# Kernel optimization log

Measured on AMD Instinct MI355X. Metric: run time of the kernel, lower is better.

Reference implementation:

```python
import jax, jax.numpy as jnp
import numpy as np
from jax import lax

DN = ('NCHW', 'OIHW', 'NCHW')

def conv2d(x, w, b):
    # valid cross-correlation, identical math to torch Conv2d / the module's
    # flattened-FFT circular-conv + roll(1) + crop trick
    y = lax.conv_general_dilated(x, w, window_strides=(1, 1), padding='VALID',
                                 dimension_numbers=DN)
    return y + b[None, :, None, None]

def max_pool2(x):
    return lax.reduce_window(x, -jnp.inf, lax.max,
                             window_dimensions=(1, 1, 2, 2),
                             window_strides=(1, 1, 2, 2), padding='VALID')

def setup_inputs() -> dict:
    key = jax.random.key(0)
    ks = jax.random.split(key, 9)
    B = 2048
    x = jax.random.normal(ks[0], (B, 1, 28, 28), dtype=jnp.float32)
    s = 0.05
    w1 = jax.random.normal(ks[1], (32, 1, 3, 3), dtype=jnp.float32) * s
    b1 = jax.random.normal(ks[2], (32,), dtype=jnp.float32) * s
    w2 = jax.random.normal(ks[3], (64, 32, 3, 3), dtype=jnp.float32) * s
    b2 = jax.random.normal(ks[4], (64,), dtype=jnp.float32) * s
    fc1_w = jax.random.normal(ks[5], (128, 9216), dtype=jnp.float32) * 0.01
    fc1_b = jax.random.normal(ks[6], (128,), dtype=jnp.float32) * s
    fc2_w = jax.random.normal(ks[7], (10, 128), dtype=jnp.float32) * s
    fc2_b = jax.random.normal(ks[8], (10,), dtype=jnp.float32) * s
    return {'x': x, 'w1': w1, 'b1': b1, 'w2': w2, 'b2': b2,
            'fc1_w': fc1_w, 'fc1_b': fc1_b, 'fc2_w': fc2_w, 'fc2_b': fc2_b}

def reference(x, w1, b1, w2, b2, fc1_w, fc1_b, fc2_w, fc2_b):
    h = jax.nn.relu(conv2d(x, w1, b1))           # [B,32,26,26]
    h = jax.nn.relu(conv2d(h, w2, b2))           # [B,64,24,24]
    h = max_pool2(h)                             # [B,64,12,12]
    # dropout layers are identity at inference
    h = h.reshape(h.shape[0], -1)                # [B,9216]
    h = jax.nn.relu(h @ fc1_w.T + fc1_b)         # [B,128]
    logits = h @ fc2_w.T + fc2_b                 # [B,10]
    # NB: original forward returns x (pre-log_softmax logits), not `output`
    return logits
```

## Files before the change

kernel.cpp:

```cpp
#include <hip/hip_runtime.h>
#include <stddef.h>


#define NIMG 2048

typedef __attribute__((ext_vector_type(8))) short short8;
typedef __attribute__((ext_vector_type(4))) float f32x4;

__device__ inline ushort f2bf(float f) {
    unsigned u = __builtin_bit_cast(unsigned, f);
    unsigned r = (u + 0x7fff + ((u >> 16) & 1)) >> 16;
    return (ushort)r;
}

__global__ void k_w2pack(const float* __restrict__ w2, ushort* __restrict__ bfr) {
    int i = blockIdx.x * 256 + threadIdx.x;
    if (i < 18432) {
        int j = i & 7;
        int l = (i >> 3) & 63;
        int t = i >> 9;
        int kyx = t % 9, nt = t / 9;
        int oc = nt * 16 + (l & 15);
        int ic = 8 * (l >> 4) + j;
        bfr[i] = f2bf(w2[oc * 288 + ic * 9 + kyx]);
    }
}

__global__ void k_fc1wpack(const float* __restrict__ fc1_w, ushort* __restrict__ wp) {
    int idx = blockIdx.x * 256 + threadIdx.x;
    if (idx < 128 * 9216) {
        int n = idx / 9216, kp = idx % 9216;
        int j = kp & 1;
        int lane = (kp >> 1) & 63;
        int t = kp >> 7;
        int i = t % 9, wv = t / 9;
        int oc = (2 * (wv & 1) + j) * 16 + (lane & 15);
        int mt = (wv >> 1) + i * 4;
        int qid = mt * 4 + (lane >> 4);
        wp[idx] = f2bf(fc1_w[(size_t)n * 9216 + oc * 144 + qid]);
    }
}

#define SWZB(q, g) ((((q) << 6) | ((g) << 4)) ^ (((q) & 14) << 3))

__launch_bounds__(512)
__global__ void k_conv_fused(const float* __restrict__ x,
                             const float* __restrict__ w1,
                             const float* __restrict__ b1,
                             const ushort* __restrict__ bfr,
                             const float* __restrict__ b2,
                             ushort* __restrict__ pooled) {
    __shared__ char smem[46400];
    float* xs = (float*)(smem + 43264);
    const int tid = threadIdx.x;
    const int img = blockIdx.x;
    const int lane = tid & 63;
    const int w = tid >> 6;

    const float* xg = x + (size_t)img * 784;
    for (int i = tid; i < 784; i += 512) xs[i] = xg[i];

    const int ocg = tid & 3;
    float w1r[72], b1r[8];
    #pragma unroll
    for (int j = 0; j < 8; j++) {
        b1r[j] = b1[ocg * 8 + j];
        #pragma unroll
        for (int q = 0; q < 9; q++) w1r[j * 9 + q] = w1[(ocg * 8 + j) * 9 + q];
    }
    __syncthreads();

    #pragma unroll
    for (int it = 0; it < 3; it++) {
        int pid = (tid >> 2) + it * 128;
        if (pid < 338) {
            int y = pid / 13;
            int px2 = (pid - y * 13) * 2;
            const float* xr = &xs[y * 28 + px2];
            float xv[3][4];
            #pragma unroll
            for (int r = 0; r < 3; r++) {
                float2 u = *(const float2*)&xr[r * 28];
                float2 v = *(const float2*)&xr[r * 28 + 2];
                xv[r][0] = u.x; xv[r][1] = u.y; xv[r][2] = v.x; xv[r][3] = v.y;
            }
            short8 pk0, pk1;
            #pragma unroll
            for (int j = 0; j < 8; j++) {
                float s0 = b1r[j], s1 = b1r[j];
                #pragma unroll
                for (int ky = 0; ky < 3; ky++)
                    #pragma unroll
                    for (int kx = 0; kx < 3; kx++) {
                        float wv = w1r[j * 9 + ky * 3 + kx];
                        s0 = fmaf(wv, xv[ky][kx], s0);
                        s1 = fmaf(wv, xv[ky][kx + 1], s1);
                    }
                pk0[j] = (short)f2bf(fmaxf(s0, 0.0f));
                pk1[j] = (short)f2bf(fmaxf(s1, 0.0f));
            }
            int pos0 = y * 26 + px2;
            *(short8*)(smem + SWZB(pos0, ocg)) = pk0;
            *(short8*)(smem + SWZB(pos0 + 1, ocg)) = pk1;
        }
    }
    __syncthreads();

    const int p = w & 1;
    const int g = w >> 1;

    short8 bf[2][9];
    #pragma unroll
    for (int j = 0; j < 2; j++)
        #pragma unroll
        for (int kyx = 0; kyx < 9; kyx++)
            bf[j][kyx] = *(const short8*)&bfr[(((2 * p + j) * 9 + kyx) * 64 + lane) * 8];

    const int row = lane & 15;
    const int ic8 = lane >> 4;
    float b2v[2];
    b2v[0] = b2[(2 * p) * 16 + row];
    b2v[1] = b2[(2 * p + 1) * 16 + row];

    unsigned* pp = (unsigned*)(pooled + (size_t)img * 9216);

    #pragma unroll 1
    for (int i = 0; i < 9; i++) {
        int mt = g + i * 4;
        int m = mt * 16 + row;
        int qid = m >> 2;
        int de = m & 3;
        int py = qid / 12, px = qid - py * 12;
        int yy = py * 2 + (de >> 1);
        int xx2 = px * 2 + (de & 1);
        int pos = yy * 26 + xx2;

        f32x4 acc0 = {0.f, 0.f, 0.f, 0.f};
        f32x4 acc1 = {0.f, 0.f, 0.f, 0.f};
        #pragma unroll
        for (int ky = 0; ky < 3; ky++)
            #pragma unroll
            for (int kx = 0; kx < 3; kx++) {
                int q = pos + ky * 26 + kx;
                short8 a = *(const short8*)(smem + SWZB(q, ic8));
                acc0 = __builtin_amdgcn_mfma_f32_16x16x32_bf16(a, bf[0][ky * 3 + kx], acc0, 0, 0, 0);
                acc1 = __builtin_amdgcn_mfma_f32_16x16x32_bf16(a, bf[1][ky * 3 + kx], acc1, 0, 0, 0);
            }
        float v0 = fmaxf(fmaxf(fmaxf(acc0[0], acc0[1]), fmaxf(acc0[2], acc0[3])) + b2v[0], 0.0f);
        float v1 = fmaxf(fmaxf(fmaxf(acc1[0], acc1[1]), fmaxf(acc1[2], acc1[3])) + b2v[1], 0.0f);
        pp[(w * 9 + i) * 64 + lane] = (unsigned)f2bf(v0) | ((unsigned)f2bf(v1) << 16);
    }
}

#define FC1_SPLIT 16
#define FC1_CHUNK 576

__launch_bounds__(512)
__global__ void k_fc1(const ushort* __restrict__ A,
                      const ushort* __restrict__ Wp,
                      float* __restrict__ part) {
    __shared__ ushort As[128 * 64];
    __shared__ ushort Ws[128 * 64];
    char* Ac = (char*)As;
    char* Wc = (char*)Ws;

    const int t = threadIdx.x;
    const int lane = t & 63;
    const int wv = t >> 6;
    const int wm = wv >> 2;
    const int wn = wv & 3;
    const int lr = lane & 15;
    const int lk = lane >> 4;
    const int m0 = blockIdx.x * 128;
    const int kc0 = blockIdx.y * FC1_CHUNK;

    const int trow = t >> 2;
    const int seg = t & 3;
    const int wb0 = trow * 128 + seg * 32;
    const int sw = (trow & 7) << 4;

    const ushort* Ab = A + (size_t)(m0 + trow) * 9216 + kc0 + seg * 16;
    const ushort* Wb = Wp + (size_t)trow * 9216 + kc0 + seg * 16;

    f32x4 acc[4][2];
    #pragma unroll
    for (int mf = 0; mf < 4; mf++)
        #pragma unroll
        for (int nf = 0; nf < 2; nf++) acc[mf][nf] = (f32x4){0.f, 0.f, 0.f, 0.f};

    short8 ra0 = *(const short8*)(Ab);
    short8 ra1 = *(const short8*)(Ab + 8);
    short8 rw0 = *(const short8*)(Wb);
    short8 rw1 = *(const short8*)(Wb + 8);
    short8 na0, na1, nw0, nw1;

    for (int s = 0; s < 9; s++) {
        *(short8*)(Ac + (wb0 ^ sw)) = ra0;
        *(short8*)(Ac + ((wb0 + 16) ^ sw)) = ra1;
        *(short8*)(Wc + (wb0 ^ sw)) = rw0;
        *(short8*)(Wc + ((wb0 + 16) ^ sw)) = rw1;
        __syncthreads();
        if (s < 8) {
            const ushort* An = Ab + (s + 1) * 64;
            const ushort* Wn = Wb + (s + 1) * 64;
            na0 = *(const short8*)(An);
            na1 = *(const short8*)(An + 8);
            nw0 = *(const short8*)(Wn);
            nw1 = *(const short8*)(Wn + 8);
        }
        #pragma unroll
        for (int ks = 0; ks < 2; ks++) {
            short8 af[4], bfr2[2];
            #pragma unroll
            for (int mf = 0; mf < 4; mf++) {
                int r = wm * 64 + mf * 16 + lr;
                af[mf] = *(const short8*)(Ac + ((r * 128 + ks * 64 + lk * 16) ^ ((r & 7) << 4)));
            }
            #pragma unroll
            for (int nf = 0; nf < 2; nf++) {
                int n = wn * 32 + nf * 16 + lr;
                bfr2[nf] = *(const short8*)(Wc + ((n * 128 + ks * 64 + lk * 16) ^ ((n & 7) << 4)));
            }
            #pragma unroll
            for (int mf = 0; mf < 4; mf++)
                #pragma unroll
                for (int nf = 0; nf < 2; nf++)
                    acc[mf][nf] = __builtin_amdgcn_mfma_f32_16x16x32_bf16(af[mf], bfr2[nf], acc[mf][nf], 0, 0, 0);
        }
        __syncthreads();
        if (s < 8) { ra0 = na0; ra1 = na1; rw0 = nw0; rw1 = nw1; }
    }

    float* pb = part + (size_t)blockIdx.y * (2048 * 128);
    #pragma unroll
    for (int mf = 0; mf < 4; mf++)
        #pragma unroll
        for (int nf = 0; nf < 2; nf++) {
            int mrow = m0 + wm * 64 + mf * 16 + lk * 4;
            int ncol = wn * 32 + nf * 16 + lr;
            #pragma unroll
            for (int q = 0; q < 4; q++)
                pb[(size_t)(mrow + q) * 128 + ncol] = acc[mf][nf][q];
        }
}

__global__ void k_fc2(const float* __restrict__ part,
                      const float* __restrict__ fc1_b,
                      const float* __restrict__ fc2_w,
                      const float* __restrict__ fc2_b,
                      float* __restrict__ out) {
    __shared__ float hs[16 * 128];
    __shared__ float wsm[10 * 128];
    __shared__ float bsm[10];
    const int t = threadIdx.x;
    const int m0 = blockIdx.x * 16;
    for (int i = t; i < 1280; i += 256) wsm[i] = fc2_w[i];
    if (t < 10) bsm[t] = fc2_b[t];
    #pragma unroll
    for (int e = 0; e < 8; e++) {
        int i = t + e * 256;
        int r = i >> 7, c = i & 127;
        float s = fc1_b[c];
        #pragma unroll
        for (int kc = 0; kc < FC1_SPLIT; kc++)
            s += part[(size_t)kc * (2048 * 128) + (size_t)(m0 + r) * 128 + c];
        hs[i] = fmaxf(s, 0.0f);
    }
    __syncthreads();
    int r = t / 16, c = t % 16;
    if (c < 10) {
        float s = bsm[c];
        const float* hp = &hs[r * 128];
        const float* wp = &wsm[c * 128];
        #pragma unroll
        for (int k = 0; k < 128; k++) s = fmaf(hp[k], wp[k], s);
        out[(size_t)(m0 + r) * 10 + c] = s;
    }
}

extern "C" void kernel_launch(void* const* d_in, const int* in_sizes, int n_in,
                              void* d_out, int out_size, void* d_ws, size_t ws_size,
                              hipStream_t stream) {
    const float* x     = (const float*)d_in[0];
    const float* w1    = (const float*)d_in[1];
    const float* b1    = (const float*)d_in[2];
    const float* w2    = (const float*)d_in[3];
    const float* b2    = (const float*)d_in[4];
    const float* fc1_w = (const float*)d_in[5];
    const float* fc1_b = (const float*)d_in[6];
    const float* fc2_w = (const float*)d_in[7];
    const float* fc2_b = (const float*)d_in[8];
    float* out = (float*)d_out;

    char* wsb = (char*)d_ws;
    ushort* bfr    = (ushort*)wsb;
    ushort* wp     = (ushort*)(wsb + 36864);
    ushort* pooled = (ushort*)(wsb + 2396160);
    float*  part   = (float*)(wsb + 40144896);

    k_w2pack<<<72, 256, 0, stream>>>(w2, bfr);
    k_fc1wpack<<<4608, 256, 0, stream>>>(fc1_w, wp);
    k_conv_fused<<<NIMG, 512, 0, stream>>>(x, w1, b1, bfr, b2, pooled);
    k_fc1<<<dim3(16, FC1_SPLIT), 512, 0, stream>>>(pooled, wp, part);
    k_fc2<<<NIMG / 16, 256, 0, stream>>>(part, fc1_b, fc2_w, fc2_b, out);
}
```

Before: 99.73 us.

## Split conv2 output tiles into sequential passes, drop LDS swizzle, raise occupancy hint

The conv2 MFMA loop now handles the two output-channel tiles one after the other instead of together, so only 9 B fragments are live at a time. This lowers VGPR pressure, and the launch bound now requests 6 blocks per SM. The first tile's pooled results are kept in a small array and packed into the output on the second pass. The XOR swizzle on the conv1 LDS layout is removed for plain linear addressing. Risks: more LDS bank conflicts, A fragments read twice, less MFMA interleaving, and `pv0[i]` indexed inside a non-unrolled loop may be placed in scratch memory. The occupancy hint may also cause spills, while LDS use alone already caps residency at about 3 blocks.

```diff
diff --git a/kernel.cpp b/kernel.cpp
--- a/kernel.cpp
+++ b/kernel.cpp
@@ -41,9 +41,7 @@
     }
 }
 
-#define SWZB(q, g) ((((q) << 6) | ((g) << 4)) ^ (((q) & 14) << 3))
-
-__launch_bounds__(512)
+__launch_bounds__(512, 6)
 __global__ void k_conv_fused(const float* __restrict__ x,
                              const float* __restrict__ w1,
                              const float* __restrict__ b1,
@@ -100,55 +98,55 @@
                 pk1[j] = (short)f2bf(fmaxf(s1, 0.0f));
             }
             int pos0 = y * 26 + px2;
-            *(short8*)(smem + SWZB(pos0, ocg)) = pk0;
-            *(short8*)(smem + SWZB(pos0 + 1, ocg)) = pk1;
+            *(short8*)(smem + pos0 * 64 + ocg * 16) = pk0;
+            *(short8*)(smem + (pos0 + 1) * 64 + ocg * 16) = pk1;
         }
     }
     __syncthreads();
 
     const int p = w & 1;
     const int g = w >> 1;
-
-    short8 bf[2][9];
-    #pragma unroll
-    for (int j = 0; j < 2; j++)
-        #pragma unroll
-        for (int kyx = 0; kyx < 9; kyx++)
-            bf[j][kyx] = *(const short8*)&bfr[(((2 * p + j) * 9 + kyx) * 64 + lane) * 8];
-
     const int row = lane & 15;
     const int ic8 = lane >> 4;
-    float b2v[2];
-    b2v[0] = b2[(2 * p) * 16 + row];
-    b2v[1] = b2[(2 * p + 1) * 16 + row];
 
     unsigned* pp = (unsigned*)(pooled + (size_t)img * 9216);
+    float pv0[9];
 
     #pragma unroll 1
-    for (int i = 0; i < 9; i++) {
-        int mt = g + i * 4;
-        int m = mt * 16 + row;
-        int qid = m >> 2;
-        int de = m & 3;
-        int py = qid / 12, px = qid - py * 12;
-        int yy = py * 2 + (de >> 1);
-        int xx2 = px * 2 + (de & 1);
-        int pos = yy * 26 + xx2;
-
-        f32x4 acc0 = {0.f, 0.f, 0.f, 0.f};
-        f32x4 acc1 = {0.f, 0.f, 0.f, 0.f};
-        #pragma unroll
-        for (int ky = 0; ky < 3; ky++)
-            #pragma unroll
-            for (int kx = 0; kx < 3; kx++) {
-                int q = pos + ky * 26 + kx;
-                short8 a = *(const short8*)(smem + SWZB(q, ic8));
-                acc0 = __builtin_amdgcn_mfma_f32_16x16x32_bf16(a, bf[0][ky * 3 + kx], acc0, 0, 0, 0);
-                acc1 = __builtin_amdgcn_mfma_f32_16x16x32_bf16(a, bf[1][ky * 3 + kx], acc1, 0, 0, 0);
-            }
-        float v0 = fmaxf(fmaxf(fmaxf(acc0[0], acc0[1]), fmaxf(acc0[2], acc0[3])) + b2v[0], 0.0f);
-        float v1 = fmaxf(fmaxf(fmaxf(acc1[0], acc1[1]), fmaxf(acc1[2], acc1[3])) + b2v[1], 0.0f);
-        pp[(w * 9 + i) * 64 + lane] = (unsigned)f2bf(v0) | ((unsigned)f2bf(v1) << 16);
+    for (int nt = 0; nt < 2; nt++) {
+        short8 bfv[9];
+        #pragma unroll
+        for (int kyx = 0; kyx < 9; kyx++)
+            bfv[kyx] = *(const short8*)&bfr[(((2 * p + nt) * 9 + kyx) * 64 + lane) * 8];
+        float b2v = b2[(2 * p + nt) * 16 + row];
+
+        #pragma unroll 1
+        for (int i = 0; i < 9; i++) {
+            int mt = g + i * 4;
+            int m = mt * 16 + row;
+            int qid = m >> 2;
+            int de = m & 3;
+            int py = qid / 12, px = qid - py * 12;
+            int yy = py * 2 + (de >> 1);
+            int xx2 = px * 2 + (de & 1);
+            const char* abase = smem + (yy * 26 + xx2) * 64 + ic8 * 16;
+
+            f32x4 acc = {0.f, 0.f, 0.f, 0.f};
+            #pragma unroll
+            for (int ky = 0; ky < 3; ky++)
+                #pragma unroll
+                for (int kx = 0; kx < 3; kx++) {
+                    short8 a = *(const short8*)(abase + (ky * 26 + kx) * 64);
+                    acc = __builtin_amdgcn_mfma_f32_16x16x32_bf16(a, bfv[ky * 3 + kx], acc, 0, 0, 0);
+                }
+            float v = fmaxf(fmaxf(fmaxf(acc[0], acc[1]), fmaxf(acc[2], acc[3])) + b2v, 0.0f);
+            if (nt == 0) {
+                pv0[i] = v;
+            } else {
+                pp[(w * 9 + i) * 64 + lane] =
+                    (unsigned)f2bf(pv0[i]) | ((unsigned)f2bf(v) << 16);
+            }
+        }
     }
 }
 
```

Result: slower. 177.8 us (+78.3%).
